# Performance work log

Measured on AMD Instinct MI355X. Metric: run time of the kernel, lower is better.

## Reference

```python
import jax, jax.numpy as jnp
import numpy as np
from jax import lax

DIM = 192
HEADS = 4
HIDDEN = int(DIM * 2.66)  # 510


def _conv1x1(x, w, b):
    # x: [B,C,H,W], w: [O,C], b: [O]
    return jnp.einsum('bchw,oc->bohw', x, w) + b[None, :, None, None]


def _dwconv3x3(x, w, b):
    # x: [B,C,H,W], w: [C,1,3,3], b: [C]
    c = x.shape[1]
    y = lax.conv_general_dilated(x, w, window_strides=(1, 1), padding='SAME',
                                 feature_group_count=c,
                                 dimension_numbers=('NCHW', 'OIHW', 'NCHW'))
    return y + b[None, :, None, None]


def _layernorm_c(x, w, b):
    # LayerNorm over channel dim (torch LayerNorm(dim) applied to b,(hw),c)
    mu = jnp.mean(x, axis=1, keepdims=True)
    var = jnp.mean((x - mu) ** 2, axis=1, keepdims=True)
    xn = (x - mu) / jnp.sqrt(var + 1e-5)
    return xn * w[None, :, None, None] + b[None, :, None, None]


def _l2norm(x):
    # F.normalize(dim=-1), eps=1e-12
    n = jnp.sqrt(jnp.sum(x * x, axis=-1, keepdims=True))
    return x / jnp.maximum(n, 1e-12)


def setup_inputs() -> dict:
    key = jax.random.key(0)
    ks = jax.random.split(key, 16)
    s = 0.02
    d, h2 = DIM, HIDDEN * 2
    return {
        'x': jax.random.normal(ks[0], (4, DIM, 128, 128), jnp.float32),
        'ln1_w': jnp.ones((d,), jnp.float32),
        'ln1_b': jnp.zeros((d,), jnp.float32),
        'qkv_w': jax.random.normal(ks[1], (3 * d, d), jnp.float32) * s,
        'qkv_b': jnp.zeros((3 * d,), jnp.float32),
        'qkv_dw_w': jax.random.normal(ks[2], (3 * d, 1, 3, 3), jnp.float32) * s,
        'qkv_dw_b': jnp.zeros((3 * d,), jnp.float32),
        'temperature': jnp.ones((HEADS, 1, 1), jnp.float32),
        'proj_w': jax.random.normal(ks[3], (d, d), jnp.float32) * s,
        'proj_b': jnp.zeros((d,), jnp.float32),
        'ln2_w': jnp.ones((d,), jnp.float32),
        'ln2_b': jnp.zeros((d,), jnp.float32),
        'pin_w': jax.random.normal(ks[4], (h2, d), jnp.float32) * s,
        'pin_b': jnp.zeros((h2,), jnp.float32),
        'dw_w': jax.random.normal(ks[5], (h2, 1, 3, 3), jnp.float32) * s,
        'dw_b': jnp.zeros((h2,), jnp.float32),
        'pout_w': jax.random.normal(ks[6], (d, HIDDEN), jnp.float32) * s,
        'pout_b': jnp.zeros((d,), jnp.float32),
    }


def _attention(x, qkv_w, qkv_b, qkv_dw_w, qkv_dw_b, temperature, proj_w, proj_b):
    b, c, h, w = x.shape
    qkv = _dwconv3x3(_conv1x1(x, qkv_w, qkv_b), qkv_dw_w, qkv_dw_b)
    q, k, v = jnp.split(qkv, 3, axis=1)
    ch = c // HEADS

    def heads(t):  # b (head c) h w -> b head c (h w)
        return t.reshape(b, HEADS, ch, h * w)

    q, k, v = heads(q), heads(k), heads(v)
    q = _l2norm(q)
    k = _l2norm(k)
    attn = jnp.einsum('bhcn,bhdn->bhcd', q, k) * temperature[None]  # [b,H,ch,ch]
    attn = jax.nn.softmax(attn, axis=-1)
    out = jnp.einsum('bhcd,bhdn->bhcn', attn, v)
    out = out.reshape(b, c, h, w)
    return _conv1x1(out, proj_w, proj_b)


def _ffn(x, pin_w, pin_b, dw_w, dw_b, pout_w, pout_b):
    y = _conv1x1(x, pin_w, pin_b)
    y = _dwconv3x3(y, dw_w, dw_b)
    x1, x2 = jnp.split(y, 2, axis=1)
    y = jax.nn.gelu(x1, approximate=False) * x2
    return _conv1x1(y, pout_w, pout_b)


def reference(x, ln1_w, ln1_b, qkv_w, qkv_b, qkv_dw_w, qkv_dw_b, temperature,
              proj_w, proj_b, ln2_w, ln2_b, pin_w, pin_b, dw_w, dw_b,
              pout_w, pout_b):
    x = x + _attention(_layernorm_c(x, ln1_w, ln1_b), qkv_w, qkv_b,
                       qkv_dw_w, qkv_dw_b, temperature, proj_w, proj_b)
    x = x + _ffn(_layernorm_c(x, ln2_w, ln2_b), pin_w, pin_b, dw_w, dw_b,
                 pout_w, pout_b)
    return x
```

## Files before the change

kernel.cpp:

```cpp
#include <hip/hip_runtime.h>
#include <math.h>

typedef long long i64;
typedef unsigned short u16;
typedef unsigned int u32;

#define HW 16384
#define DIM 192
#define NHEADS 4
#define CH 48
#define OQKV 576
#define HID 510
#define H2 1020
#define NB 4
#define NSPLIT 64
#define QKPAD 132

typedef __attribute__((ext_vector_type(8))) short short8v;
typedef __attribute__((ext_vector_type(4))) float float4v;

__device__ __forceinline__ u16 f2bf(float f) {
  union { float f; u32 u; } v; v.f = f;
  u32 r = v.u + 0x7FFF + ((v.u >> 16) & 1);
  return (u16)(r >> 16);
}
__device__ __forceinline__ float bflo(u32 w) {
  union { u32 u; float f; } v; v.u = w << 16; return v.f;
}
__device__ __forceinline__ float bfhi(u32 w) {
  union { u32 u; float f; } v; v.u = w & 0xFFFF0000u; return v.f;
}
__device__ __forceinline__ float bf1(u16 h) {
  union { u32 u; float f; } v; v.u = ((u32)h) << 16; return v.f;
}
__device__ __forceinline__ u32 pk(float a, float b) {
  return (u32)f2bf(a) | ((u32)f2bf(b) << 16);
}
__device__ __forceinline__ float gelu_s(float x) {
  return x / (1.f + __expf(-1.702f * x));
}

#define GLL16(gp, lp) __builtin_amdgcn_global_load_lds( \
    (const __attribute__((address_space(1))) u32*)(gp), \
    (__attribute__((address_space(3))) u32*)(lp), 16, 0, 0)

__global__ __launch_bounds__(256) void ln_kernel(const float* __restrict__ x,
    const float* __restrict__ w, const float* __restrict__ b, u16* __restrict__ yT) {
  __shared__ float st[32][193];
  __shared__ float red[2][8][32];
  __shared__ float murs[2][32];
  const float* xb = x + (i64)blockIdx.y * DIM * HW;
  u16* yb = yT + (i64)blockIdx.y * (i64)HW * DIM;
  int tid = threadIdx.x;
  int g = tid >> 5, p = tid & 31;
  int pix0 = blockIdx.x * 32;
  float s = 0.f, ss = 0.f;
  #pragma unroll
  for (int i = 0; i < 24; ++i) {
    float t = xb[(i64)(g * 24 + i) * HW + pix0 + p];
    st[p][g * 24 + i] = t; s += t; ss += t * t;
  }
  red[0][g][p] = s; red[1][g][p] = ss;
  __syncthreads();
  if (tid < 32) {
    float S = 0.f, SS = 0.f;
    #pragma unroll
    for (int gg = 0; gg < 8; ++gg) { S += red[0][gg][tid]; SS += red[1][gg][tid]; }
    float mu = S * (1.f / DIM);
    float var = SS * (1.f / DIM) - mu * mu;
    murs[0][tid] = mu;
    murs[1][tid] = rsqrtf(var + 1e-5f);
  }
  __syncthreads();
  int px = tid >> 3, c0 = (tid & 7) * 24;
  float mu = murs[0][px], rs = murs[1][px];
  u16 ob[24];
  #pragma unroll
  for (int i = 0; i < 24; ++i) {
    ob[i] = f2bf((st[px][c0 + i] - mu) * rs * w[c0 + i] + b[c0 + i]);
  }
  u16* yp = yb + (i64)(pix0 + px) * DIM + c0;
  #pragma unroll
  for (int j = 0; j < 3; ++j) *(uint4*)(yp + j * 8) = *(const uint4*)&ob[j * 8];
}

__global__ __launch_bounds__(256) void wconv_all(const float* __restrict__ qkv_w,
    const float* __restrict__ proj_w, const float* __restrict__ pin_w,
    const float* __restrict__ pout_w, u16* __restrict__ Wq, u16* __restrict__ Wpj,
    u16* __restrict__ Wpi, u16* __restrict__ Wpo) {
  int idx = blockIdx.x * 256 + threadIdx.x;
  const float* src; u16* dst; int O, C, Kpad;
  if (idx < 122880)      { src = qkv_w;  dst = Wq;  O = OQKV; C = 192; Kpad = 192; }
  else if (idx < 172032) { idx -= 122880; src = proj_w; dst = Wpj; O = 192;  C = 192; Kpad = 192; }
  else if (idx < 368640) { idx -= 172032; src = pin_w;  dst = Wpi; O = H2;   C = 192; Kpad = 192; }
  else if (idx < 499712) { idx -= 368640; src = pout_w; dst = Wpo; O = 192;  C = HID; Kpad = 512; }
  else return;
  int r = idx / Kpad, c = idx - r * Kpad;
  dst[idx] = f2bf((r < O && c < C) ? src[(i64)r * C + c] : 0.f);
}

__global__ __launch_bounds__(256) void gemm_bf16(const u16* __restrict__ A,
    const float* __restrict__ bias, const u16* __restrict__ B,
    const float* __restrict__ Res, float* __restrict__ Out,
    u16* __restrict__ OutB, int O, int K, i64 sB, i64 sOut, i64 sRes) {
  __shared__ __align__(16) u16 lds[2 * 128 * 64];
  int zb = blockIdx.z;
  B += (i64)zb * sB;
  if (Res) Res += (i64)zb * sRes;
  if (OutB) OutB += (i64)zb * sOut; else Out += (i64)zb * sOut;
  int tid = threadIdx.x;
  int lane = tid & 63, wave = tid >> 6;
  int wm = (wave >> 1) * 64, wn = (wave & 1) * 64;
  int obase = blockIdx.y * 128, nbase = blockIdx.x * 128;
  float4v acc[4][4];
  #pragma unroll
  for (int m = 0; m < 4; ++m)
    #pragma unroll
    for (int n = 0; n < 4; ++n) acc[m][n] = (float4v){0.f, 0.f, 0.f, 0.f};

  const u16* Abase = A + (i64)obase * K;
  const u16* Bbase = B + (i64)nbase * K;
  char* ldsA = (char*)&lds[0];
  char* ldsB = (char*)&lds[8192];
  int srow = wave * 8 + (lane >> 3);
  int sj = lane & 7;

  for (int k0 = 0; k0 < K; k0 += 64) {
    #pragma unroll
    for (int iss = 0; iss < 4; ++iss) {
      int r = iss * 32 + srow;
      int kb = sj ^ (r & 7);
      GLL16(Abase + (i64)r * K + k0 + kb * 8, ldsA + iss * 4096 + wave * 1024);
      GLL16(Bbase + (i64)r * K + k0 + kb * 8, ldsB + iss * 4096 + wave * 1024);
    }
    __syncthreads();
    #pragma unroll
    for (int kk = 0; kk < 2; ++kk) {
      short8v af[4], bfr[4];
      #pragma unroll
      for (int m = 0; m < 4; ++m) {
        int r = wm + m * 16 + (lane & 15);
        int kb = kk * 4 + (lane >> 4);
        af[m] = *(const short8v*)(ldsA + r * 128 + ((kb ^ (r & 7)) << 4));
      }
      #pragma unroll
      for (int n = 0; n < 4; ++n) {
        int r = wn + n * 16 + (lane & 15);
        int kb = kk * 4 + (lane >> 4);
        bfr[n] = *(const short8v*)(ldsB + r * 128 + ((kb ^ (r & 7)) << 4));
      }
      #pragma unroll
      for (int m = 0; m < 4; ++m)
        #pragma unroll
        for (int n = 0; n < 4; ++n)
          acc[m][n] = __builtin_amdgcn_mfma_f32_16x16x32_bf16(af[m], bfr[n], acc[m][n], 0, 0, 0);
    }
    __syncthreads();
  }

  int rowq = lane >> 4, coln = lane & 15;
  if (OutB) {
    #pragma unroll
    for (int m = 0; m < 4; ++m) {
      #pragma unroll
      for (int reg = 0; reg < 4; ++reg) {
        int o = wm + m * 16 + rowq * 4 + reg;
        int oo = obase + o;
        float bv = (oo < O) ? bias[oo] : 0.f;
        #pragma unroll
        for (int n = 0; n < 4; ++n) {
          lds[o * 128 + wn + n * 16 + coln] = f2bf(acc[m][n][reg] + bv);
        }
      }
    }
    __syncthreads();
    const u32* st32 = (const u32*)lds;
    #pragma unroll
    for (int k = 0; k < 32; ++k) {
      int idx = k * 256 + tid;
      int o = idx >> 6, cd = idx & 63;
      if (obase + o < O)
        ((u32*)(OutB + (i64)(obase + o) * HW + nbase))[cd] = st32[o * 64 + cd];
    }
  } else {
    #pragma unroll
    for (int m = 0; m < 4; ++m) {
      #pragma unroll
      for (int reg = 0; reg < 4; ++reg) {
        int o = obase + wm + m * 16 + rowq * 4 + reg;
        if (o >= O) continue;
        float bv = bias[o];
        #pragma unroll
        for (int n = 0; n < 4; ++n) {
          int nn = nbase + wn + n * 16 + coln;
          float v = acc[m][n][reg] + bv;
          if (Res) v += Res[(i64)o * HW + nn];
          Out[(i64)o * HW + nn] = v;
        }
      }
    }
  }
}

__global__ __launch_bounds__(256) void dwconv_bf16(const u16* __restrict__ in,
    const float* __restrict__ w9, const float* __restrict__ bs,
    u16* __restrict__ out) {
  in  += (i64)blockIdx.z * OQKV * HW;
  out += (i64)blockIdx.z * OQKV * HW;
  int q = threadIdx.x & 31;
  int grp = threadIdx.x >> 5;
  int y0 = blockIdx.y * 2;
  int c0 = blockIdx.x * 64 + grp * 8;
  int xb = q * 4;
  #pragma unroll
  for (int i = 0; i < 8; ++i) {
    int c = c0 + i;
    const float* wp = w9 + c * 9;
    float bv = bs[c];
    const u16* chan = in + (i64)c * HW;
    float f[4][6];
    #pragma unroll
    for (int r4 = 0; r4 < 4; ++r4) {
      int yy = y0 - 1 + r4;
      if (yy < 0 || yy >= 128) {
        #pragma unroll
        for (int e = 0; e < 6; ++e) f[r4][e] = 0.f;
      } else {
        uint4 raw = *(const uint4*)(chan + yy * 128 + xb - 2);
        f[r4][0] = (q == 0) ? 0.f : bfhi(raw.x);
        f[r4][1] = bflo(raw.y); f[r4][2] = bfhi(raw.y);
        f[r4][3] = bflo(raw.z); f[r4][4] = bfhi(raw.z);
        f[r4][5] = (q == 31) ? 0.f : bflo(raw.w);
      }
    }
    #pragma unroll
    for (int rr = 0; rr < 2; ++rr) {
      float a0 = bv, a1 = bv, a2 = bv, a3 = bv;
      #pragma unroll
      for (int dy = 0; dy < 3; ++dy) {
        float wa = wp[dy * 3 + 0], wb = wp[dy * 3 + 1], wc = wp[dy * 3 + 2];
        const float* fr = f[rr + dy];
        a0 += wa * fr[0] + wb * fr[1] + wc * fr[2];
        a1 += wa * fr[1] + wb * fr[2] + wc * fr[3];
        a2 += wa * fr[2] + wb * fr[3] + wc * fr[4];
        a3 += wa * fr[3] + wb * fr[4] + wc * fr[5];
      }
      ushort4 o;
      o.x = f2bf(a0); o.y = f2bf(a1); o.z = f2bf(a2); o.w = f2bf(a3);
      *(ushort4*)(out + (i64)c * HW + (y0 + rr) * 128 + xb) = o;
    }
  }
}

__global__ __launch_bounds__(256) void attn_qk_kernel(const u16* __restrict__ qkv,
    float* __restrict__ part, float* __restrict__ partN) {
  qkv   += (i64)blockIdx.z * OQKV * HW;
  part  += (i64)blockIdx.z * 589824;
  partN += (i64)blockIdx.z * 24576;
  __shared__ float qs[48][QKPAD];
  __shared__ float ks[48][QKPAD];
  int h = blockIdx.x, sp = blockIdx.y;
  int n0 = sp * (HW / NSPLIT);
  const u16* qb = qkv + (i64)(h * CH) * HW + n0;
  const u16* kb = qkv + (i64)(DIM + h * CH) * HW + n0;
  int tid = threadIdx.x;
  int c0 = (tid >> 4) * 3, d0 = (tid & 15) * 3;
  bool isq = (tid & 15) == 0;
  bool isk = (tid >> 4) == 0;
  float acc[3][3] = {};
  float qn[3] = {}, kn[3] = {};
  for (int nn = 0; nn < 256; nn += 128) {
    for (int l = tid; l < 48 * 16; l += 256) {
      int r = l >> 4, j = (l & 15) * 8;
      uint4 rq = *(const uint4*)(qb + (i64)r * HW + nn + j);
      uint4 rk = *(const uint4*)(kb + (i64)r * HW + nn + j);
      qs[r][j + 0] = bflo(rq.x); qs[r][j + 1] = bfhi(rq.x);
      qs[r][j + 2] = bflo(rq.y); qs[r][j + 3] = bfhi(rq.y);
      qs[r][j + 4] = bflo(rq.z); qs[r][j + 5] = bfhi(rq.z);
      qs[r][j + 6] = bflo(rq.w); qs[r][j + 7] = bfhi(rq.w);
      ks[r][j + 0] = bflo(rk.x); ks[r][j + 1] = bfhi(rk.x);
      ks[r][j + 2] = bflo(rk.y); ks[r][j + 3] = bfhi(rk.y);
      ks[r][j + 4] = bflo(rk.z); ks[r][j + 5] = bfhi(rk.z);
      ks[r][j + 6] = bflo(rk.w); ks[r][j + 7] = bfhi(rk.w);
    }
    __syncthreads();
    #pragma unroll 2
    for (int j = 0; j < 128; j += 4) {
      float qv[3][4], kv[3][4];
      #pragma unroll
      for (int i = 0; i < 3; ++i) {
        float4 t = *(const float4*)&qs[c0 + i][j];
        qv[i][0] = t.x; qv[i][1] = t.y; qv[i][2] = t.z; qv[i][3] = t.w;
        float4 u = *(const float4*)&ks[d0 + i][j];
        kv[i][0] = u.x; kv[i][1] = u.y; kv[i][2] = u.z; kv[i][3] = u.w;
      }
      #pragma unroll
      for (int i = 0; i < 3; ++i)
        #pragma unroll
        for (int jj = 0; jj < 3; ++jj)
          #pragma unroll
          for (int e = 0; e < 4; ++e)
            acc[i][jj] += qv[i][e] * kv[jj][e];
      if (isq) {
        #pragma unroll
        for (int i = 0; i < 3; ++i)
          #pragma unroll
          for (int e = 0; e < 4; ++e) qn[i] += qv[i][e] * qv[i][e];
      }
      if (isk) {
        #pragma unroll
        for (int i = 0; i < 3; ++i)
          #pragma unroll
          for (int e = 0; e < 4; ++e) kn[i] += kv[i][e] * kv[i][e];
      }
    }
    __syncthreads();
  }
  float* pp = part + ((i64)(h * NSPLIT) + sp) * 2304;
  #pragma unroll
  for (int i = 0; i < 3; ++i)
    #pragma unroll
    for (int jj = 0; jj < 3; ++jj)
      pp[(c0 + i) * 48 + d0 + jj] = acc[i][jj];
  float* pn = partN + ((i64)(h * NSPLIT) + sp) * 96;
  if (isq) {
    #pragma unroll
    for (int i = 0; i < 3; ++i) pn[c0 + i] = qn[i];
  }
  if (isk) {
    #pragma unroll
    for (int i = 0; i < 3; ++i) pn[48 + d0 + i] = kn[i];
  }
}

__global__ __launch_bounds__(64) void attn_sm3(const float* __restrict__ part,
    const float* __restrict__ partN, const float* __restrict__ temp,
    float* __restrict__ attn) {
  part  += (i64)blockIdx.z * 589824;
  partN += (i64)blockIdx.z * 24576;
  attn  += (i64)blockIdx.z * 9216;
  int h = blockIdx.x, c = blockIdx.y;
  int d = threadIdx.x;
  const float* pN = partN + (i64)h * NSPLIT * 96;
  float sq = pN[d * 96 + c];
  #pragma unroll
  for (int mask = 32; mask; mask >>= 1) sq += __shfl_xor(sq, mask);
  float invq = 1.f / fmaxf(sqrtf(sq), 1e-12f);
  float logit = -1e30f;
  if (d < CH) {
    float sk = 0.f, s = 0.f;
    for (int sp = 0; sp < NSPLIT; ++sp) {
      sk += pN[sp * 96 + 48 + d];
      s += part[((i64)(h * NSPLIT) + sp) * 2304 + c * 48 + d];
    }
    float invk = 1.f / fmaxf(sqrtf(sk), 1e-12f);
    logit = s * invq * invk * temp[h];
  }
  float m = logit;
  #pragma unroll
  for (int mask = 32; mask; mask >>= 1) m = fmaxf(m, __shfl_xor(m, mask));
  float e = (d < CH) ? expf(logit - m) : 0.f;
  float ssum = e;
  #pragma unroll
  for (int mask = 32; mask; mask >>= 1) ssum += __shfl_xor(ssum, mask);
  if (d < CH) attn[(i64)h * 2304 + c * 48 + d] = e / ssum;
}

__global__ __launch_bounds__(256) void attn_v_kernel(const u16* __restrict__ qkv,
    const float* __restrict__ attnm, u16* __restrict__ outT) {
  qkv   += (i64)blockIdx.z * OQKV * HW;
  attnm += (i64)blockIdx.z * 9216;
  outT  += (i64)blockIdx.z * (i64)HW * DIM;
  __shared__ float as[CH * CH];
  __shared__ u16 st[256 * 52];
  int h = blockIdx.x, tile = blockIdx.y;
  int tid = threadIdx.x;
  for (int l = tid; l < CH * CH; l += 256) as[l] = attnm[(i64)h * 2304 + l];
  __syncthreads();
  int n = tile * 256 + tid;
  const u16* vb = qkv + (i64)(2 * DIM + h * CH) * HW + n;
  float vreg[CH];
  #pragma unroll
  for (int d = 0; d < CH; ++d) vreg[d] = bf1(vb[(i64)d * HW]);
  u32* strow = (u32*)st + tid * 26;
  #pragma unroll 2
  for (int c = 0; c < CH; c += 4) {
    float a0 = 0.f, a1 = 0.f, a2 = 0.f, a3 = 0.f;
    const float* r0 = &as[(c + 0) * CH];
    const float* r1 = &as[(c + 1) * CH];
    const float* r2 = &as[(c + 2) * CH];
    const float* r3 = &as[(c + 3) * CH];
    #pragma unroll
    for (int d = 0; d < CH; ++d) {
      float vv = vreg[d];
      a0 += r0[d] * vv; a1 += r1[d] * vv; a2 += r2[d] * vv; a3 += r3[d] * vv;
    }
    strow[(c >> 1) + 0] = pk(a0, a1);
    strow[(c >> 1) + 1] = pk(a2, a3);
  }
  __syncthreads();
  const uint2* sv = (const uint2*)st;
  u16* ob = outT + (i64)(tile * 256) * DIM + h * CH;
  #pragma unroll
  for (int k = 0; k < 12; ++k) {
    int idx = k * 256 + tid;
    int px = idx / 12, pc = idx - px * 12;
    *(uint2*)(ob + (i64)px * DIM + pc * 4) = sv[px * 13 + pc];
  }
}

__global__ __launch_bounds__(256) void dwgate_bf16(const u16* __restrict__ h1,
    const float* __restrict__ w9, const float* __restrict__ bs,
    u16* __restrict__ og) {
  h1 += (i64)blockIdx.z * H2 * HW;
  og += (i64)blockIdx.z * (i64)HW * 512;
  __shared__ u32 st[128 * 33];
  int q = threadIdx.x & 31;
  int grp = threadIdx.x >> 5;
  int y = blockIdx.y;
  int c0 = blockIdx.x * 64 + grp * 8;
  int xb = q * 4;
  float res[4][8];
  #pragma unroll
  for (int i = 0; i < 8; ++i) {
    int c = c0 + i;
    bool valid = (c < HID);
    float b1 = valid ? bs[c] : 0.f;
    float b2 = valid ? bs[c + HID] : 0.f;
    float a0 = b1, a1 = b1, a2 = b1, a3 = b1;
    float g0 = b2, g1 = b2, g2 = b2, g3 = b2;
    if (valid) {
      const float* wp1 = w9 + c * 9;
      const float* wp2 = w9 + (i64)(c + HID) * 9;
      const u16* ch1 = h1 + (i64)c * HW;
      const u16* ch2 = h1 + (i64)(c + HID) * HW;
      #pragma unroll
      for (int dy = -1; dy <= 1; ++dy) {
        int yy = y + dy;
        if (yy < 0 || yy >= 128) continue;
        {
          uint4 raw = *(const uint4*)(ch1 + yy * 128 + xb - 2);
          float f1 = bfhi(raw.x);
          float f2 = bflo(raw.y), f3 = bfhi(raw.y);
          float f4 = bflo(raw.z), f5 = bfhi(raw.z);
          float f6 = bflo(raw.w);
          if (q == 0) f1 = 0.f;
          if (q == 31) f6 = 0.f;
          float wa = wp1[(dy + 1) * 3 + 0], wb = wp1[(dy + 1) * 3 + 1], wc = wp1[(dy + 1) * 3 + 2];
          a0 += wa * f1 + wb * f2 + wc * f3;
          a1 += wa * f2 + wb * f3 + wc * f4;
          a2 += wa * f3 + wb * f4 + wc * f5;
          a3 += wa * f4 + wb * f5 + wc * f6;
        }
        {
          uint4 raw = *(const uint4*)(ch2 + yy * 128 + xb - 2);
          float f1 = bfhi(raw.x);
          float f2 = bflo(raw.y), f3 = bfhi(raw.y);
          float f4 = bflo(raw.z), f5 = bfhi(raw.z);
          float f6 = bflo(raw.w);
          if (q == 0) f1 = 0.f;
          if (q == 31) f6 = 0.f;
          float wa = wp2[(dy + 1) * 3 + 0], wb = wp2[(dy + 1) * 3 + 1], wc = wp2[(dy + 1) * 3 + 2];
          g0 += wa * f1 + wb * f2 + wc * f3;
          g1 += wa * f2 + wb * f3 + wc * f4;
          g2 += wa * f3 + wb * f4 + wc * f5;
          g3 += wa * f4 + wb * f5 + wc * f6;
        }
      }
    }
    res[0][i] = valid ? gelu_s(a0) * g0 : 0.f;
    res[1][i] = valid ? gelu_s(a1) * g1 : 0.f;
    res[2][i] = valid ? gelu_s(a2) * g2 : 0.f;
    res[3][i] = valid ? gelu_s(a3) * g3 : 0.f;
  }
  #pragma unroll
  for (int j = 0; j < 4; ++j) {
    int px = xb + j;
    u32* row = st + px * 33 + grp * 4;
    row[0] = pk(res[j][0], res[j][1]);
    row[1] = pk(res[j][2], res[j][3]);
    row[2] = pk(res[j][4], res[j][5]);
    row[3] = pk(res[j][6], res[j][7]);
  }
  __syncthreads();
  u32* og32 = (u32*)og;
  int tid = threadIdx.x;
  #pragma unroll
  for (int k = 0; k < 16; ++k) {
    int idx = k * 256 + tid;
    int px = idx >> 5, dwi = idx & 31;
    og32[(i64)(y * 128 + px) * 256 + blockIdx.x * 32 + dwi] = st[px * 33 + dwi];
  }
}

extern "C" void kernel_launch(void* const* d_in, const int* in_sizes, int n_in,
                              void* d_out, int out_size, void* d_ws, size_t ws_size,
                              hipStream_t stream) {
  const float* x        = (const float*)d_in[0];
  const float* ln1_w    = (const float*)d_in[1];
  const float* ln1_b    = (const float*)d_in[2];
  const float* qkv_w    = (const float*)d_in[3];
  const float* qkv_b    = (const float*)d_in[4];
  const float* qkv_dw_w = (const float*)d_in[5];
  const float* qkv_dw_b = (const float*)d_in[6];
  const float* temp     = (const float*)d_in[7];
  const float* proj_w   = (const float*)d_in[8];
  const float* proj_b   = (const float*)d_in[9];
  const float* ln2_w    = (const float*)d_in[10];
  const float* ln2_b    = (const float*)d_in[11];
  const float* pin_w    = (const float*)d_in[12];
  const float* pin_b    = (const float*)d_in[13];
  const float* dw_w     = (const float*)d_in[14];
  const float* dw_b     = (const float*)d_in[15];
  const float* pout_w   = (const float*)d_in[16];
  const float* pout_b   = (const float*)d_in[17];
  float* out = (float*)d_out;
  char* ws = (char*)d_ws;

  u16* Wq   = (u16*)ws;
  u16* Wpj  = Wq + 640 * 192;
  u16* Wpi  = Wpj + 256 * 192;
  u16* Wpo  = Wpi + 1024 * 192;
  u16* yT   = Wpo + 256 * 512;
  char* dyn = (char*)(yT + (i64)NB * HW * DIM);

  auto layout = [&](int nb, float*& attnm, float*& part, float*& partN,
                    u16*& bufA, u16*& bufQ) -> size_t {
    char* p = dyn;
    attnm = (float*)p; p += (i64)nb * 9216 * 4;
    part  = (float*)p; p += (i64)nb * 589824 * 4;
    partN = (float*)p; p += (i64)nb * 24576 * 4;
    bufA  = (u16*)p;   p += (i64)nb * H2 * HW * 2;
    bufQ  = (u16*)p;   p += (i64)nb * OQKV * HW * 2;
    return (size_t)(p - ws);
  };

  float *attnm, *part, *partN; u16 *bufA, *bufQ;
  int nbat = 4;
  if (layout(4, attnm, part, partN, bufA, bufQ) > ws_size) {
    nbat = 1;
    if (layout(1, attnm, part, partN, bufA, bufQ) > ws_size) return;
  }

  wconv_all<<<(499712 + 255) / 256, 256, 0, stream>>>(qkv_w, proj_w, pin_w, pout_w,
                                                      Wq, Wpj, Wpi, Wpo);
  ln_kernel<<<dim3(HW / 32, NB), 256, 0, stream>>>(x, ln1_w, ln1_b, yT);

  for (int b0 = 0; b0 < NB; b0 += nbat) {
    const float* xb = x + (i64)b0 * DIM * HW;
    float* outb = out + (i64)b0 * DIM * HW;
    u16* yTb = yT + (i64)b0 * HW * DIM;
    u16* attnoutT = bufA;
    u16* gatedT = bufQ;

    gemm_bf16<<<dim3(HW / 128, 5, nbat), 256, 0, stream>>>(
        Wq, qkv_b, yTb, nullptr, nullptr, bufA, OQKV, DIM,
        (i64)HW * DIM, (i64)OQKV * HW, 0);
    dwconv_bf16<<<dim3(OQKV / 64, 64, nbat), 256, 0, stream>>>(bufA, qkv_dw_w, qkv_dw_b, bufQ);
    attn_qk_kernel<<<dim3(NHEADS, NSPLIT, nbat), 256, 0, stream>>>(bufQ, part, partN);
    attn_sm3<<<dim3(NHEADS, CH, nbat), 64, 0, stream>>>(part, partN, temp, attnm);
    attn_v_kernel<<<dim3(NHEADS, HW / 256, nbat), 256, 0, stream>>>(bufQ, attnm, attnoutT);
    gemm_bf16<<<dim3(HW / 128, 2, nbat), 256, 0, stream>>>(
        Wpj, proj_b, attnoutT, xb, outb, nullptr, DIM, DIM,
        (i64)HW * DIM, (i64)DIM * HW, (i64)DIM * HW);

    ln_kernel<<<dim3(HW / 32, nbat), 256, 0, stream>>>(outb, ln2_w, ln2_b, yTb);
    gemm_bf16<<<dim3(HW / 128, 8, nbat), 256, 0, stream>>>(
        Wpi, pin_b, yTb, nullptr, nullptr, bufA, H2, DIM,
        (i64)HW * DIM, (i64)H2 * HW, 0);
    dwgate_bf16<<<dim3(8, 128, nbat), 256, 0, stream>>>(bufA, dw_w, dw_b, gatedT);
    gemm_bf16<<<dim3(HW / 128, 2, nbat), 256, 0, stream>>>(
        Wpo, pout_b, gatedT, outb, outb, nullptr, DIM, 512,
        (i64)HW * 512, (i64)DIM * HW, (i64)DIM * HW);
  }
}
```

Before: 513.3 us.

## Compute Q·K^T partial Gram matrices with bf16 MFMA and separate L2-norm kernel

```diff
diff --git a/kernel.cpp b/kernel.cpp
--- a/kernel.cpp
+++ b/kernel.cpp
@@ -14,7 +14,7 @@
 #define H2 1020
 #define NB 4
 #define NSPLIT 64
-#define QKPAD 132
+#define QKSTR 264
 
 typedef __attribute__((ext_vector_type(8))) short short8v;
 typedef __attribute__((ext_vector_type(4))) float float4v;
@@ -252,109 +252,102 @@
   }
 }
 
-__global__ __launch_bounds__(256) void attn_qk_kernel(const u16* __restrict__ qkv,
-    float* __restrict__ part, float* __restrict__ partN) {
-  qkv   += (i64)blockIdx.z * OQKV * HW;
-  part  += (i64)blockIdx.z * 589824;
-  partN += (i64)blockIdx.z * 24576;
-  __shared__ float qs[48][QKPAD];
-  __shared__ float ks[48][QKPAD];
-  int h = blockIdx.x, sp = blockIdx.y;
-  int n0 = sp * (HW / NSPLIT);
-  const u16* qb = qkv + (i64)(h * CH) * HW + n0;
-  const u16* kb = qkv + (i64)(DIM + h * CH) * HW + n0;
+__global__ __launch_bounds__(256) void l2inv_bf16(const u16* __restrict__ qkv,
+    float* __restrict__ inv) {
+  int ch = blockIdx.x;
+  const u16* p = qkv + (i64)blockIdx.y * OQKV * HW + (i64)ch * HW;
+  float s = 0.f;
+  for (int i = threadIdx.x * 8; i < HW; i += 256 * 8) {
+    uint4 raw = *(const uint4*)(p + i);
+    float v0 = bflo(raw.x), v1 = bfhi(raw.x);
+    float v2 = bflo(raw.y), v3 = bfhi(raw.y);
+    float v4 = bflo(raw.z), v5 = bfhi(raw.z);
+    float v6 = bflo(raw.w), v7 = bfhi(raw.w);
+    s += v0 * v0 + v1 * v1 + v2 * v2 + v3 * v3 + v4 * v4 + v5 * v5 + v6 * v6 + v7 * v7;
+  }
+  #pragma unroll
+  for (int m = 32; m; m >>= 1) s += __shfl_xor(s, m);
+  __shared__ float wsum[4];
+  int lane = threadIdx.x & 63, wid = threadIdx.x >> 6;
+  if (lane == 0) wsum[wid] = s;
+  __syncthreads();
+  if (threadIdx.x == 0) {
+    float t = wsum[0] + wsum[1] + wsum[2] + wsum[3];
+    inv[(i64)blockIdx.y * 384 + ch] = 1.f / fmaxf(sqrtf(t), 1e-12f);
+  }
+}
+
+__global__ __launch_bounds__(256) void attn_qk_mfma(const u16* __restrict__ qkv,
+    float* __restrict__ part) {
+  qkv  += (i64)blockIdx.z * OQKV * HW;
+  part += (i64)blockIdx.z * 589824;
+  __shared__ __align__(16) u16 qs[48][QKSTR];
+  __shared__ __align__(16) u16 ks[48][QKSTR];
+  int h = blockIdx.x, spb = blockIdx.y;
+  int n0 = spb * 1024;
+  const u16* qb = qkv + (i64)(h * CH) * HW;
+  const u16* kb = qkv + (i64)(DIM + h * CH) * HW;
   int tid = threadIdx.x;
-  int c0 = (tid >> 4) * 3, d0 = (tid & 15) * 3;
-  bool isq = (tid & 15) == 0;
-  bool isk = (tid >> 4) == 0;
-  float acc[3][3] = {};
-  float qn[3] = {}, kn[3] = {};
-  for (int nn = 0; nn < 256; nn += 128) {
-    for (int l = tid; l < 48 * 16; l += 256) {
-      int r = l >> 4, j = (l & 15) * 8;
-      uint4 rq = *(const uint4*)(qb + (i64)r * HW + nn + j);
-      uint4 rk = *(const uint4*)(kb + (i64)r * HW + nn + j);
-      qs[r][j + 0] = bflo(rq.x); qs[r][j + 1] = bfhi(rq.x);
-      qs[r][j + 2] = bflo(rq.y); qs[r][j + 3] = bfhi(rq.y);
-      qs[r][j + 4] = bflo(rq.z); qs[r][j + 5] = bfhi(rq.z);
-      qs[r][j + 6] = bflo(rq.w); qs[r][j + 7] = bfhi(rq.w);
-      ks[r][j + 0] = bflo(rk.x); ks[r][j + 1] = bfhi(rk.x);
-      ks[r][j + 2] = bflo(rk.y); ks[r][j + 3] = bfhi(rk.y);
-      ks[r][j + 4] = bflo(rk.z); ks[r][j + 5] = bfhi(rk.z);
-      ks[r][j + 6] = bflo(rk.w); ks[r][j + 7] = bfhi(rk.w);
+  int lane = tid & 63, wave = tid >> 6;
+  float4v acc[3][3];
+  #pragma unroll
+  for (int i = 0; i < 3; ++i)
+    #pragma unroll
+    for (int j = 0; j < 3; ++j) acc[i][j] = (float4v){0.f, 0.f, 0.f, 0.f};
+
+  for (int it = 0; it < 4; ++it) {
+    int base = n0 + it * 256;
+    for (int l = tid; l < 1536; l += 256) {
+      int r = l >> 5, j = (l & 31) * 8;
+      *(uint4*)&qs[r][j] = *(const uint4*)(qb + (i64)r * HW + base + j);
+      *(uint4*)&ks[r][j] = *(const uint4*)(kb + (i64)r * HW + base + j);
     }
     __syncthreads();
-    #pragma unroll 2
-    for (int j = 0; j < 128; j += 4) {
-      float qv[3][4], kv[3][4];
-      #pragma unroll
-      for (int i = 0; i < 3; ++i) {
-        float4 t = *(const float4*)&qs[c0 + i][j];
-        qv[i][0] = t.x; qv[i][1] = t.y; qv[i][2] = t.z; qv[i][3] = t.w;
-        float4 u = *(const float4*)&ks[d0 + i][j];
-        kv[i][0] = u.x; kv[i][1] = u.y; kv[i][2] = u.z; kv[i][3] = u.w;
-      }
-      #pragma unroll
-      for (int i = 0; i < 3; ++i)
+    int kbase = wave * 64;
+    #pragma unroll
+    for (int ksi = 0; ksi < 2; ++ksi) {
+      int kofs = kbase + ksi * 32 + (lane >> 4) * 8;
+      short8v aq[3], bk[3];
+      #pragma unroll
+      for (int t = 0; t < 3; ++t) {
+        aq[t] = *(const short8v*)&qs[t * 16 + (lane & 15)][kofs];
+        bk[t] = *(const short8v*)&ks[t * 16 + (lane & 15)][kofs];
+      }
+      #pragma unroll
+      for (int ci = 0; ci < 3; ++ci)
         #pragma unroll
-        for (int jj = 0; jj < 3; ++jj)
-          #pragma unroll
-          for (int e = 0; e < 4; ++e)
-            acc[i][jj] += qv[i][e] * kv[jj][e];
-      if (isq) {
-        #pragma unroll
-        for (int i = 0; i < 3; ++i)
-          #pragma unroll
-          for (int e = 0; e < 4; ++e) qn[i] += qv[i][e] * qv[i][e];
-      }
-      if (isk) {
-        #pragma unroll
-        for (int i = 0; i < 3; ++i)
-          #pragma unroll
-          for (int e = 0; e < 4; ++e) kn[i] += kv[i][e] * kv[i][e];
-      }
+        for (int di = 0; di < 3; ++di)
+          acc[ci][di] = __builtin_amdgcn_mfma_f32_16x16x32_bf16(aq[ci], bk[di], acc[ci][di], 0, 0, 0);
     }
     __syncthreads();
   }
-  float* pp = part + ((i64)(h * NSPLIT) + sp) * 2304;
-  #pragma unroll
-  for (int i = 0; i < 3; ++i)
-    #pragma unroll
-    for (int jj = 0; jj < 3; ++jj)
-      pp[(c0 + i) * 48 + d0 + jj] = acc[i][jj];
-  float* pn = partN + ((i64)(h * NSPLIT) + sp) * 96;
-  if (isq) {
-    #pragma unroll
-    for (int i = 0; i < 3; ++i) pn[c0 + i] = qn[i];
-  }
-  if (isk) {
-    #pragma unroll
-    for (int i = 0; i < 3; ++i) pn[48 + d0 + i] = kn[i];
-  }
+  int rowq = lane >> 4, coln = lane & 15;
+  float* pp = part + ((i64)(h * NSPLIT) + spb * 4 + wave) * 2304;
+  #pragma unroll
+  for (int ci = 0; ci < 3; ++ci)
+    #pragma unroll
+    for (int reg = 0; reg < 4; ++reg) {
+      int c = ci * 16 + rowq * 4 + reg;
+      #pragma unroll
+      for (int di = 0; di < 3; ++di)
+        pp[c * 48 + di * 16 + coln] = acc[ci][di][reg];
+    }
 }
 
 __global__ __launch_bounds__(64) void attn_sm3(const float* __restrict__ part,
-    const float* __restrict__ partN, const float* __restrict__ temp,
+    const float* __restrict__ inv, const float* __restrict__ temp,
     float* __restrict__ attn) {
-  part  += (i64)blockIdx.z * 589824;
-  partN += (i64)blockIdx.z * 24576;
-  attn  += (i64)blockIdx.z * 9216;
+  part += (i64)blockIdx.z * 589824;
+  attn += (i64)blockIdx.z * 9216;
+  const float* invb = inv + (i64)blockIdx.z * 384;
   int h = blockIdx.x, c = blockIdx.y;
   int d = threadIdx.x;
-  const float* pN = partN + (i64)h * NSPLIT * 96;
-  float sq = pN[d * 96 + c];
-  #pragma unroll
-  for (int mask = 32; mask; mask >>= 1) sq += __shfl_xor(sq, mask);
-  float invq = 1.f / fmaxf(sqrtf(sq), 1e-12f);
   float logit = -1e30f;
   if (d < CH) {
-    float sk = 0.f, s = 0.f;
-    for (int sp = 0; sp < NSPLIT; ++sp) {
-      sk += pN[sp * 96 + 48 + d];
+    float s = 0.f;
+    for (int sp = 0; sp < NSPLIT; ++sp)
       s += part[((i64)(h * NSPLIT) + sp) * 2304 + c * 48 + d];
-    }
-    float invk = 1.f / fmaxf(sqrtf(sk), 1e-12f);
-    logit = s * invq * invk * temp[h];
+    logit = s * invb[h * CH + c] * invb[192 + h * CH + d] * temp[h];
   }
   float m = logit;
   #pragma unroll
@@ -524,22 +517,22 @@
   u16* yT   = Wpo + 256 * 512;
   char* dyn = (char*)(yT + (i64)NB * HW * DIM);
 
-  auto layout = [&](int nb, float*& attnm, float*& part, float*& partN,
+  auto layout = [&](int nb, float*& attnm, float*& part, float*& invv,
                     u16*& bufA, u16*& bufQ) -> size_t {
     char* p = dyn;
     attnm = (float*)p; p += (i64)nb * 9216 * 4;
     part  = (float*)p; p += (i64)nb * 589824 * 4;
-    partN = (float*)p; p += (i64)nb * 24576 * 4;
+    invv  = (float*)p; p += (i64)nb * 384 * 4;
     bufA  = (u16*)p;   p += (i64)nb * H2 * HW * 2;
     bufQ  = (u16*)p;   p += (i64)nb * OQKV * HW * 2;
     return (size_t)(p - ws);
   };
 
-  float *attnm, *part, *partN; u16 *bufA, *bufQ;
+  float *attnm, *part, *invv; u16 *bufA, *bufQ;
   int nbat = 4;
-  if (layout(4, attnm, part, partN, bufA, bufQ) > ws_size) {
+  if (layout(4, attnm, part, invv, bufA, bufQ) > ws_size) {
     nbat = 1;
-    if (layout(1, attnm, part, partN, bufA, bufQ) > ws_size) return;
+    if (layout(1, attnm, part, invv, bufA, bufQ) > ws_size) return;
   }
 
   wconv_all<<<(499712 + 255) / 256, 256, 0, stream>>>(qkv_w, proj_w, pin_w, pout_w,
@@ -557,8 +550,9 @@
         Wq, qkv_b, yTb, nullptr, nullptr, bufA, OQKV, DIM,
         (i64)HW * DIM, (i64)OQKV * HW, 0);
     dwconv_bf16<<<dim3(OQKV / 64, 64, nbat), 256, 0, stream>>>(bufA, qkv_dw_w, qkv_dw_b, bufQ);
-    attn_qk_kernel<<<dim3(NHEADS, NSPLIT, nbat), 256, 0, stream>>>(bufQ, part, partN);
-    attn_sm3<<<dim3(NHEADS, CH, nbat), 64, 0, stream>>>(part, partN, temp, attnm);
+    l2inv_bf16<<<dim3(384, nbat), 256, 0, stream>>>(bufQ, invv);
+    attn_qk_mfma<<<dim3(NHEADS, 16, nbat), 256, 0, stream>>>(bufQ, part);
+    attn_sm3<<<dim3(NHEADS, CH, nbat), 64, 0, stream>>>(part, invv, temp, attnm);
     attn_v_kernel<<<dim3(NHEADS, HW / 256, nbat), 256, 0, stream>>>(bufQ, attnm, attnoutT);
     gemm_bf16<<<dim3(HW / 128, 2, nbat), 256, 0, stream>>>(
         Wpj, proj_b, attnoutT, xb, outb, nullptr, DIM, DIM,
```

After: 501.6 us. 1.02x faster.
